# Optimization experiments

Measured on AMD Instinct MI355X. Metric: run time of the kernel, lower is better.

The kernel has to match this reference:

```python
import jax, jax.numpy as jnp
import numpy as np

B, N = 4, 32768
IN_CH, OUT_CH, SD = 4, 4, 3
WIDTH, DEPTH, M, H, FFN = 256, 8, 32, 8, 1024
CF, TF, FB = 8, 4, 1000
IN_DIM = IN_CH + 2 * CF + 2 * TF  # 28
DH = WIDTH // H


def setup_inputs() -> dict:
    key = jax.random.key(0)
    ks = jax.random.split(key, 16)
    r = lambda i, shape, s=0.02: jax.random.normal(ks[i], shape, dtype=jnp.float32) * s
    return {
        "features": jax.random.normal(ks[0], (B, N, IN_CH), dtype=jnp.float32),
        "coords": jax.random.uniform(ks[1], (B, N, SD), minval=-1.0, maxval=1.0),
        "t_norm": jax.random.uniform(ks[2], (B,)),
        "freq_matrix": jax.random.normal(ks[3], (SD, CF), dtype=jnp.float32),
        "omega": FB ** (-jnp.arange(TF, dtype=jnp.float32) / TF),
        "in_w": r(4, (IN_DIM, WIDTH)), "in_b": jnp.zeros((WIDTH,)),
        "ln1_g": jnp.ones((DEPTH, WIDTH)), "ln1_b": jnp.zeros((DEPTH, WIDTH)),
        "slice_w": r(5, (DEPTH, WIDTH, M)), "slice_b": jnp.zeros((DEPTH, M)),
        "qkv_w": r(6, (DEPTH, WIDTH, 3 * WIDTH)), "qkv_b": jnp.zeros((DEPTH, 3 * WIDTH)),
        "attn_out_w": r(7, (DEPTH, WIDTH, WIDTH)), "attn_out_b": jnp.zeros((DEPTH, WIDTH)),
        "ln2_g": jnp.ones((DEPTH, WIDTH)), "ln2_b": jnp.zeros((DEPTH, WIDTH)),
        "ffn1_w": r(8, (DEPTH, WIDTH, FFN)), "ffn1_b": jnp.zeros((DEPTH, FFN)),
        "ffn2_w": r(9, (DEPTH, FFN, WIDTH)), "ffn2_b": jnp.zeros((DEPTH, WIDTH)),
        "out_w": r(10, (WIDTH, OUT_CH)), "out_b": jnp.zeros((OUT_CH,)),
    }


def _ln(x, g, b):
    mu = x.mean(-1, keepdims=True)
    var = ((x - mu) ** 2).mean(-1, keepdims=True)
    return (x - mu) * jax.lax.rsqrt(var + 1e-5) * g + b


def _mha(z, qkv_w, qkv_b, ow, ob):
    # z: (B, M, WIDTH). Standard torch nn.MultiheadAttention self-attn.
    qkv = z @ qkv_w + qkv_b                      # (B, M, 3*WIDTH)
    q, k, v = jnp.split(qkv, 3, axis=-1)
    sh = (z.shape[0], M, H, DH)
    q = q.reshape(sh).transpose(0, 2, 1, 3)      # (B, H, M, DH)
    k = k.reshape(sh).transpose(0, 2, 1, 3)
    v = v.reshape(sh).transpose(0, 2, 1, 3)
    scores = jnp.einsum('bhmd,bhkd->bhmk', q, k) / jnp.sqrt(jnp.float32(DH))
    attn = jax.nn.softmax(scores, axis=-1)
    o = jnp.einsum('bhmk,bhkd->bhmd', attn, v)   # (B, H, M, DH)
    o = o.transpose(0, 2, 1, 3).reshape(z.shape[0], M, WIDTH)
    return o @ ow + ob


def _physics_attention(h, sw, sb, qkv_w, qkv_b, ow, ob):
    # h: (B, N, WIDTH)
    w = jax.nn.softmax(h @ sw + sb, axis=-1)                 # (B, N, M)
    wsum = jnp.clip(w.sum(axis=1), 1e-8, None)               # (B, M)
    slices = jnp.einsum('bnm,bnd->bmd', w, h) / wsum[..., None]
    slices_out = _mha(slices, qkv_w, qkv_b, ow, ob)          # (B, M, WIDTH)
    return jnp.einsum('bnm,bmd->bnd', w, slices_out)         # (B, N, WIDTH)


def _forward(features, coords, t_norm, freq_matrix, omega, in_w, in_b,
             ln1_g, ln1_b, slice_w, slice_b, qkv_w, qkv_b, attn_out_w, attn_out_b,
             ln2_g, ln2_b, ffn1_w, ffn1_b, ffn2_w, ffn2_b, out_w, out_b):
    # Spatial LFF encoding
    proj = 2.0 * jnp.pi * (coords @ freq_matrix)             # (B, N, CF)
    sp = jnp.concatenate([jnp.sin(proj), jnp.cos(proj)], axis=-1)
    # Temporal sinusoidal encoding, broadcast to all nodes
    angles = omega[None, :] * (t_norm * FB)[:, None]         # (B, TF)
    te = jnp.concatenate([jnp.sin(angles), jnp.cos(angles)], axis=-1)
    te = jnp.broadcast_to(te[:, None, :], (features.shape[0], features.shape[1], 2 * TF))
    x = jnp.concatenate([features, sp, te], axis=-1) @ in_w + in_b  # (B, N, WIDTH)
    for i in range(DEPTH):
        h = _ln(x, ln1_g[i], ln1_b[i])
        x = x + _physics_attention(h, slice_w[i], slice_b[i], qkv_w[i], qkv_b[i],
                                   attn_out_w[i], attn_out_b[i])
        h2 = _ln(x, ln2_g[i], ln2_b[i])
        x = x + jax.nn.gelu(h2 @ ffn1_w[i] + ffn1_b[i], approximate=False) @ ffn2_w[i] + ffn2_b[i]
    return x @ out_w + out_b                                 # (B, N, OUT_CH)


def reference(features, coords, t_norm, freq_matrix, omega, in_w, in_b,
              ln1_g, ln1_b, slice_w, slice_b, qkv_w, qkv_b, attn_out_w, attn_out_b,
              ln2_g, ln2_b, ffn1_w, ffn1_b, ffn2_w, ffn2_b, out_w, out_b):
    return _forward(features, coords, t_norm, freq_matrix, omega, in_w, in_b,
                    ln1_g, ln1_b, slice_w, slice_b, qkv_w, qkv_b, attn_out_w, attn_out_b,
                    ln2_g, ln2_b, ffn1_w, ffn1_b, ffn2_w, ffn2_b, out_w, out_b)
```

## Files before the change

### kernel.cpp

```cpp
#include <hip/hip_runtime.h>

#define BB 4
#define NN 32768
#define BN 131072
#define WD 256
#define NDEPTH 8
#define MS 32
#define NH 8
#define DHD 32
#define FF 1024

typedef float f32x4 __attribute__((ext_vector_type(4)));
typedef float f32x2 __attribute__((ext_vector_type(2)));
typedef _Float16 f16x8 __attribute__((ext_vector_type(8)));
typedef _Float16 f16x4 __attribute__((ext_vector_type(4)));

__device__ __forceinline__ float rcp_(float x){ return __builtin_amdgcn_rcpf(x); }
__device__ __forceinline__ float rsq_(float x){ return __builtin_amdgcn_rsqf(x); }

__device__ __forceinline__ float gelu_f(float x){
  float z  = 0.70710678118654752f * x;
  float az = fabsf(z);
  float t  = rcp_(fmaf(0.3275911f, az, 1.0f));
  float p  = fmaf(t, 1.061405429f, -1.453152027f);
  p = fmaf(t, p, 1.421413741f);
  p = fmaf(t, p, -0.284496736f);
  p = fmaf(t, p, 0.254829592f);
  p = p * t;
  float e  = __expf(-az*az);
  float er = 1.0f - p*e;
  er = (z < 0.0f) ? -er : er;
  return 0.5f * x * (1.0f + er);
}

__global__ __launch_bounds__(256) void k_prep_w1t(const float* __restrict__ f1w,
                                                  const float* __restrict__ ln2g,
                                                  _Float16* __restrict__ W1T){
  int id = blockIdx.x*256 + threadIdx.x;
  int k = id & 255; int f = (id >> 8) & 1023; int i = id >> 18;
  W1T[id] = (_Float16)(ln2g[i*256+k] * f1w[(size_t)i*262144 + (size_t)k*1024 + f]);
}
__global__ __launch_bounds__(256) void k_prep_w2t(const float* __restrict__ f2w,
                                                  _Float16* __restrict__ W2T){
  int id = blockIdx.x*256 + threadIdx.x;
  int k = id & 1023; int n = (id >> 10) & 255; int i = id >> 18;
  W2T[id] = (_Float16)(f2w[(size_t)i*262144 + (size_t)k*256 + n]);
}
__global__ __launch_bounds__(256) void k_prep_s1c1(const float* __restrict__ f1w,
                                                   const float* __restrict__ ln2g,
                                                   const float* __restrict__ ln2b,
                                                   const float* __restrict__ f1b,
                                                   float* __restrict__ S1, float* __restrict__ C1){
  int fb = blockIdx.x; int i = blockIdx.y; int t = threadIdx.x;
  int f = fb*256 + t;
  const float* w = f1w + (size_t)i*262144 + f;
  float s = 0.f, c = 0.f;
  for (int k = 0; k < 256; ++k){
    float wv = w[(size_t)k*1024];
    s = fmaf(ln2g[i*256+k], wv, s);
    c = fmaf(ln2b[i*256+k], wv, c);
  }
  S1[i*1024+f] = s;
  C1[i*1024+f] = c + f1b[i*1024+f];
}
__global__ __launch_bounds__(256) void k_prep_qkvt(const float* __restrict__ qkvw,
                                                   float* __restrict__ qkvwT){
  int id = blockIdx.x*256 + threadIdx.x;
  int d = id & 255; int cl = id >> 8;
  int c = cl % 768; int L = cl / 768;
  qkvwT[id] = qkvw[(size_t)L*196608 + (size_t)d*768 + c];
}

__global__ __launch_bounds__(256) void k_encode(const float* __restrict__ feat,
                                                const float* __restrict__ coords,
                                                const float* __restrict__ tn,
                                                const float* __restrict__ fm,
                                                const float* __restrict__ om,
                                                const float* __restrict__ in_w,
                                                const float* __restrict__ in_b,
                                                float* __restrict__ X){
  __shared__ float inw[28*256];
  __shared__ float enc[8][28];
  int t = threadIdx.x;
  for (int i = 0; i < 28; ++i) inw[i*256+t] = in_w[i*256+t];
  float bv = in_b[t];
  int row0 = blockIdx.x * 128;
  __syncthreads();
  for (int it = 0; it < 16; ++it){
    int rbase = row0 + it*8;
    if (t < 224){
      int rr = t / 28, j = t - rr*28;
      int row = rbase + rr; int b = row >> 15;
      float v;
      if (j < 4){
        v = feat[(size_t)row*4 + j];
      } else if (j < 20){
        int fi = (j - 4) & 7;
        const float* cp = coords + (size_t)row*3;
        float pr = 6.2831853071795864f * (cp[0]*fm[fi] + cp[1]*fm[8+fi] + cp[2]*fm[16+fi]);
        v = (j < 12) ? sinf(pr) : cosf(pr);
      } else {
        int fi = (j - 20) & 3;
        float ang = om[fi] * (tn[b] * 1000.0f);
        v = (j < 24) ? sinf(ang) : cosf(ang);
      }
      enc[rr][j] = v;
    }
    __syncthreads();
    for (int rr = 0; rr < 8; ++rr){
      float a = bv;
      #pragma unroll 7
      for (int j = 0; j < 28; ++j) a = fmaf(enc[rr][j], inw[j*256+t], a);
      X[(size_t)(rbase+rr)*256 + t] = a;
    }
    __syncthreads();
  }
}

__global__ __launch_bounds__(256) void k_slice(const float* __restrict__ X,
                                               float* __restrict__ Wb,
                                               float* __restrict__ S,
                                               float* __restrict__ WS,
                                               const float* __restrict__ swp,
                                               const float* __restrict__ sbp,
                                               const float* __restrict__ g1p,
                                               const float* __restrict__ b1p){
  __shared__ float hl[4][256];
  __shared__ float part[4][256];
  __shared__ float wl[4][32];
  __shared__ float red[4][8];
  int t = threadIdx.x;
  int base = (t >> 5) << 5;
  int m = t & 31;
  float swreg[32];
  #pragma unroll
  for (int j = 0; j < 32; ++j) swreg[j] = swp[(size_t)(base+j)*32 + m];
  float g1 = g1p[t], b1 = b1p[t];
  float sbv = sbp[t & 31];
  float acc[32];
  #pragma unroll
  for (int i = 0; i < 32; ++i) acc[i] = 0.f;
  float wacc = 0.f;
  int row0 = blockIdx.x * 128;
  int b = row0 >> 15;
  int wv_id = t >> 6;
  for (int it = 0; it < 32; ++it){
    int rb = row0 + it*4;
    float xv[4], sm[4], qm[4];
    #pragma unroll
    for (int r = 0; r < 4; ++r) xv[r] = X[(size_t)(rb+r)*256 + t];
    #pragma unroll
    for (int r = 0; r < 4; ++r){ sm[r] = xv[r]; qm[r] = xv[r]*xv[r]; }
    #pragma unroll
    for (int off = 32; off; off >>= 1){
      #pragma unroll
      for (int r = 0; r < 4; ++r){ sm[r] += __shfl_xor(sm[r], off); qm[r] += __shfl_xor(qm[r], off); }
    }
    if ((t & 63) == 0){
      #pragma unroll
      for (int r = 0; r < 4; ++r){ red[r][wv_id*2] = sm[r]; red[r][wv_id*2+1] = qm[r]; }
    }
    __syncthreads();
    float h[4];
    #pragma unroll
    for (int r = 0; r < 4; ++r){
      float sum = red[r][0]+red[r][2]+red[r][4]+red[r][6];
      float sq  = red[r][1]+red[r][3]+red[r][5]+red[r][7];
      float mu  = sum * (1.f/256.f);
      float var = sq * (1.f/256.f) - mu*mu;
      float rstd = rsq_(var + 1e-5f);
      h[r] = (xv[r] - mu)*rstd*g1 + b1;
      hl[r][t] = h[r];
    }
    __syncthreads();
    #pragma unroll
    for (int r = 0; r < 4; ++r){
      float p = 0.f;
      #pragma unroll
      for (int j = 0; j < 32; ++j) p = fmaf(hl[r][base+j], swreg[j], p);
      part[r][t] = p;
    }
    __syncthreads();
    if (t < 128){
      int r = t >> 5, mm = t & 31;
      float lg = sbv;
      #pragma unroll
      for (int g = 0; g < 8; ++g) lg += part[r][g*32 + mm];
      float mx = lg;
      #pragma unroll
      for (int off = 16; off; off >>= 1) mx = fmaxf(mx, __shfl_xor(mx, off));
      float e = __expf(lg - mx);
      float se = e;
      #pragma unroll
      for (int off = 16; off; off >>= 1) se += __shfl_xor(se, off);
      float wv = e * rcp_(se);
      wl[r][mm] = wv;
      Wb[(size_t)(rb+r)*32 + mm] = wv;
      wacc += wv;
    }
    __syncthreads();
    #pragma unroll
    for (int r = 0; r < 4; ++r)
      #pragma unroll
      for (int i = 0; i < 32; ++i) acc[i] = fmaf(wl[r][i], h[r], acc[i]);
  }
  #pragma unroll 8
  for (int i = 0; i < 32; ++i) atomicAdd(&S[(size_t)(b*32+i)*256 + t], acc[i]);
  if (t < 128) ((float*)hl)[t] = wacc;
  __syncthreads();
  if (t < 32){
    float* f = (float*)hl;
    atomicAdd(&WS[b*32 + t], f[t] + f[32+t] + f[64+t] + f[96+t]);
  }
}

__global__ __launch_bounds__(256) void k_mha(const float* __restrict__ S,
                                             const float* __restrict__ WS,
                                             float* __restrict__ O,
                                             const float* __restrict__ qkvwT,
                                             const float* __restrict__ qkvb){
  __shared__ float zl[32*256];
  __shared__ float qkl[3][32][33];
  __shared__ float att[32][33];
  __shared__ float wsl[32];
  int t = threadIdx.x;
  int b = blockIdx.x >> 3, h = blockIdx.x & 7;
  if (t < 32) wsl[t] = rcp_(fmaxf(WS[b*32+t], 1e-8f));
  __syncthreads();
  #pragma unroll
  for (int i = 0; i < 8; ++i){
    int idx = i*1024 + t*4;
    int mm = idx >> 8; int d = idx & 255;
    f32x4 v = *reinterpret_cast<const f32x4*>(S + (size_t)(b*32+mm)*256 + d);
    v *= wsl[mm];
    *reinterpret_cast<f32x4*>(&zl[idx]) = v;
  }
  __syncthreads();
  for (int i = 0; i < 12; ++i){
    int o = i*256 + t;
    int which = o >> 10, rem = o & 1023, mm = rem >> 5, dh = rem & 31;
    int col = which*256 + h*32 + dh;
    const f32x4* zp = reinterpret_cast<const f32x4*>(&zl[mm*256]);
    const f32x4* wp = reinterpret_cast<const f32x4*>(qkvwT + (size_t)col*256);
    f32x4 av = {0.f,0.f,0.f,0.f};
    #pragma unroll 8
    for (int d4 = 0; d4 < 64; ++d4) av += zp[d4]*wp[d4];
    qkl[which][mm][dh] = av[0]+av[1]+av[2]+av[3] + qkvb[col];
  }
  __syncthreads();
  for (int i = 0; i < 4; ++i){
    int e = i*256 + t; int mm = e >> 5; int k2 = e & 31;
    float a = 0.f;
    #pragma unroll 8
    for (int d = 0; d < 32; ++d) a = fmaf(qkl[0][mm][d], qkl[1][k2][d], a);
    att[mm][k2] = a * 0.17677669529663687f;
  }
  __syncthreads();
  {
    int mm = t >> 3, j = t & 7;
    float v0 = att[mm][j], v1 = att[mm][j+8], v2 = att[mm][j+16], v3 = att[mm][j+24];
    float mx = fmaxf(fmaxf(v0, v1), fmaxf(v2, v3));
    #pragma unroll
    for (int off = 4; off; off >>= 1) mx = fmaxf(mx, __shfl_xor(mx, off));
    v0 = __expf(v0-mx); v1 = __expf(v1-mx); v2 = __expf(v2-mx); v3 = __expf(v3-mx);
    float sm = v0+v1+v2+v3;
    #pragma unroll
    for (int off = 4; off; off >>= 1) sm += __shfl_xor(sm, off);
    float inv = rcp_(sm);
    att[mm][j] = v0*inv; att[mm][j+8] = v1*inv; att[mm][j+16] = v2*inv; att[mm][j+24] = v3*inv;
  }
  __syncthreads();
  for (int i = 0; i < 4; ++i){
    int e = i*256 + t; int mm = e >> 5; int dh = e & 31;
    float a = 0.f;
    #pragma unroll 8
    for (int k2 = 0; k2 < 32; ++k2) a = fmaf(att[mm][k2], qkl[2][k2][dh], a);
    O[(size_t)(b*32+mm)*256 + h*32 + dh] = a;
  }
}

__global__ __launch_bounds__(256) void k_outproj(const float* __restrict__ O,
                                                 float* __restrict__ SO,
                                                 const float* __restrict__ aow,
                                                 const float* __restrict__ aob){
  __shared__ float orow[256];
  int t = threadIdx.x; int row = blockIdx.x;
  orow[t] = O[(size_t)row*256 + t];
  __syncthreads();
  float a = aob[t];
  #pragma unroll 4
  for (int d = 0; d < 256; ++d) a = fmaf(orow[d], aow[(size_t)d*256 + t], a);
  SO[(size_t)row*256 + t] = a;
}

__global__ __launch_bounds__(256) void k_deslice(float* __restrict__ X,
                                                 const float* __restrict__ Wb,
                                                 const float* __restrict__ SO,
                                                 float* __restrict__ ST){
  __shared__ float wrow[4][32];
  __shared__ float red[4][8];
  int t = threadIdx.x;
  int row0 = blockIdx.x * 32;
  int b = row0 >> 15;
  int wv_id = t >> 6;
  float soc[32];
  #pragma unroll 8
  for (int i = 0; i < 32; ++i) soc[i] = SO[(size_t)(b*32+i)*256 + t];
  for (int it = 0; it < 8; ++it){
    int rb = row0 + it*4;
    if (t < 128) wrow[t>>5][t&31] = Wb[(size_t)(rb + (t>>5))*32 + (t&31)];
    __syncthreads();
    float xn[4], sm[4], qm[4];
    #pragma unroll
    for (int r = 0; r < 4; ++r){
      float xv = X[(size_t)(rb+r)*256 + t];
      float dv = 0.f;
      #pragma unroll
      for (int i = 0; i < 32; ++i) dv = fmaf(wrow[r][i], soc[i], dv);
      xn[r] = xv + dv;
      X[(size_t)(rb+r)*256 + t] = xn[r];
      sm[r] = xn[r]; qm[r] = xn[r]*xn[r];
    }
    #pragma unroll
    for (int off = 32; off; off >>= 1){
      #pragma unroll
      for (int r = 0; r < 4; ++r){ sm[r] += __shfl_xor(sm[r], off); qm[r] += __shfl_xor(qm[r], off); }
    }
    if ((t & 63) == 0){
      #pragma unroll
      for (int r = 0; r < 4; ++r){ red[r][wv_id*2] = sm[r]; red[r][wv_id*2+1] = qm[r]; }
    }
    __syncthreads();
    if (t < 4){
      int r = t;
      float sum = red[r][0]+red[r][2]+red[r][4]+red[r][6];
      float sq  = red[r][1]+red[r][3]+red[r][5]+red[r][7];
      float mu  = sum * (1.f/256.f);
      float var = sq * (1.f/256.f) - mu*mu;
      float rstd = rsq_(var + 1e-5f);
      ST[(size_t)(rb+r)*2]   = rstd;
      ST[(size_t)(rb+r)*2+1] = rstd*mu;
    }
  }
}

__global__ __launch_bounds__(256) void k_ffn1(const float* __restrict__ X,
                                              const _Float16* __restrict__ W1T,
                                              const float* __restrict__ S1,
                                              const float* __restrict__ C1,
                                              const float* __restrict__ ST,
                                              _Float16* __restrict__ U, int c0){
  __shared__ _Float16 As[128*40];
  __shared__ _Float16 Bs[128*40];
  __shared__ f32x2 stl[128];
  int t = threadIdx.x;
  int nb = blockIdx.x;
  int my = blockIdx.y;
  int row0 = c0 + my*128;
  int w = t >> 6, l = t & 63;
  int wm = w >> 1, wn = w & 1, lr = l & 15, lk = l >> 4;
  f32x4 acc[4][4] = {};
  for (int ks = 0; ks < 8; ++ks){
    int k0 = ks*32;
    {
      int r = t >> 3, qd = t & 7;
      #pragma unroll
      for (int i = 0; i < 4; ++i){
        int rr = i*32 + r;
        f32x4 v = *reinterpret_cast<const f32x4*>(X + (size_t)(row0+rr)*256 + k0 + qd*4);
        f16x4 hv; hv[0]=(_Float16)v[0]; hv[1]=(_Float16)v[1]; hv[2]=(_Float16)v[2]; hv[3]=(_Float16)v[3];
        *reinterpret_cast<f16x4*>(&As[rr*40 + qd*4]) = hv;
      }
      #pragma unroll
      for (int i = 0; i < 2; ++i){
        int e = i*256 + t; int fr = e >> 2; int qb = e & 3;
        f16x8 hv = *reinterpret_cast<const f16x8*>(W1T + (size_t)(nb*128+fr)*256 + k0 + qb*8);
        *reinterpret_cast<f16x8*>(&Bs[fr*40 + qb*8]) = hv;
      }
    }
    __syncthreads();
    f16x8 a[4], bf[4];
    #pragma unroll
    for (int i = 0; i < 4; ++i) a[i]  = *reinterpret_cast<const f16x8*>(&As[(64*wm + 16*i + lr)*40 + lk*8]);
    #pragma unroll
    for (int i = 0; i < 4; ++i) bf[i] = *reinterpret_cast<const f16x8*>(&Bs[(64*wn + 16*i + lr)*40 + lk*8]);
    #pragma unroll
    for (int mt = 0; mt < 4; ++mt)
      #pragma unroll
      for (int nt = 0; nt < 4; ++nt)
        acc[mt][nt] = __builtin_amdgcn_mfma_f32_16x16x32_f16(a[mt], bf[nt], acc[mt][nt], 0, 0, 0);
    __syncthreads();
  }
  if (t < 128) stl[t] = *reinterpret_cast<const f32x2*>(ST + (size_t)(row0+t)*2);
  __syncthreads();
  #pragma unroll
  for (int nt = 0; nt < 4; ++nt){
    int f = nb*128 + 64*wn + 16*nt + lr;
    float s1 = S1[f], c1 = C1[f];
    #pragma unroll
    for (int mt = 0; mt < 4; ++mt){
      int lrow0 = 64*wm + 16*mt + lk*4;
      #pragma unroll
      for (int e = 0; e < 4; ++e){
        f32x2 st2 = stl[lrow0 + e];
        float u = st2[0]*acc[mt][nt][e] - st2[1]*s1 + c1;
        U[(size_t)(my*128 + lrow0 + e)*1024 + f] = (_Float16)gelu_f(u);
      }
    }
  }
}

__global__ __launch_bounds__(256) void k_ffn2(const _Float16* __restrict__ U,
                                              const _Float16* __restrict__ W2T,
                                              const float* __restrict__ f2b,
                                              float* __restrict__ X, int c0){
  __shared__ _Float16 As[128*40];
  __shared__ _Float16 Bs[128*40];
  int t = threadIdx.x;
  int nb = blockIdx.x;
  int my = blockIdx.y;
  int w = t >> 6, l = t & 63;
  int wm = w >> 1, wn = w & 1, lr = l & 15, lk = l >> 4;
  f32x4 acc[4][4] = {};
  for (int ks = 0; ks < 32; ++ks){
    int k0 = ks*32;
    #pragma unroll
    for (int i = 0; i < 2; ++i){
      int e = i*256 + t; int r = e >> 2; int qb = e & 3;
      f16x8 hv  = *reinterpret_cast<const f16x8*>(U   + (size_t)(my*128+r)*1024 + k0 + qb*8);
      *reinterpret_cast<f16x8*>(&As[r*40 + qb*8]) = hv;
      f16x8 hv2 = *reinterpret_cast<const f16x8*>(W2T + (size_t)(nb*128+r)*1024 + k0 + qb*8);
      *reinterpret_cast<f16x8*>(&Bs[r*40 + qb*8]) = hv2;
    }
    __syncthreads();
    f16x8 a[4], bf[4];
    #pragma unroll
    for (int i = 0; i < 4; ++i) a[i]  = *reinterpret_cast<const f16x8*>(&As[(64*wm + 16*i + lr)*40 + lk*8]);
    #pragma unroll
    for (int i = 0; i < 4; ++i) bf[i] = *reinterpret_cast<const f16x8*>(&Bs[(64*wn + 16*i + lr)*40 + lk*8]);
    #pragma unroll
    for (int mt = 0; mt < 4; ++mt)
      #pragma unroll
      for (int nt = 0; nt < 4; ++nt)
        acc[mt][nt] = __builtin_amdgcn_mfma_f32_16x16x32_f16(a[mt], bf[nt], acc[mt][nt], 0, 0, 0);
    __syncthreads();
  }
  #pragma unroll
  for (int nt = 0; nt < 4; ++nt){
    int c = nb*128 + 64*wn + 16*nt + lr;
    float bv = f2b[c];
    #pragma unroll
    for (int mt = 0; mt < 4; ++mt){
      int gr = c0 + my*128 + 64*wm + 16*mt + lk*4;
      #pragma unroll
      for (int e = 0; e < 4; ++e){
        size_t idx = (size_t)(gr+e)*256 + c;
        X[idx] = X[idx] + acc[mt][nt][e] + bv;
      }
    }
  }
}

__global__ __launch_bounds__(256) void k_final(const float* __restrict__ X,
                                               const float* __restrict__ out_w,
                                               const float* __restrict__ out_b,
                                               float* __restrict__ out){
  int t = threadIdx.x; int w = t >> 6; int l = t & 63;
  f32x4 ow[4];
  #pragma unroll
  for (int j = 0; j < 4; ++j) ow[j] = *reinterpret_cast<const f32x4*>(out_w + (4*l+j)*4);
  f32x4 ob = *reinterpret_cast<const f32x4*>(out_b);
  int row0 = blockIdx.x * 256;
  for (int it = 0; it < 64; ++it){
    int row = row0 + it*4 + w;
    f32x4 xv = *reinterpret_cast<const f32x4*>(X + (size_t)row*256 + 4*l);
    f32x4 p = ow[0]*xv[0];
    p += ow[1]*xv[1]; p += ow[2]*xv[2]; p += ow[3]*xv[3];
    #pragma unroll
    for (int off = 32; off; off >>= 1){
      p[0] += __shfl_xor(p[0], off);
      p[1] += __shfl_xor(p[1], off);
      p[2] += __shfl_xor(p[2], off);
      p[3] += __shfl_xor(p[3], off);
    }
    if (l == 0) *reinterpret_cast<f32x4*>(out + (size_t)row*4) = p + ob;
  }
}

static constexpr size_t OFF_X   = 0;
static constexpr size_t SZ_X    = (size_t)BN*256*4;
static constexpr size_t OFF_W   = OFF_X + SZ_X;
static constexpr size_t SZ_W    = (size_t)BN*32*4;
static constexpr size_t OFF_ST  = OFF_W + SZ_W;
static constexpr size_t SZ_ST   = (size_t)BN*2*4;
static constexpr size_t OFF_S   = OFF_ST + SZ_ST;
static constexpr size_t SZ_S    = (size_t)4*32*256*4;
static constexpr size_t OFF_WS  = OFF_S + SZ_S;
static constexpr size_t OFF_O   = OFF_WS + 1024;
static constexpr size_t OFF_SO  = OFF_O + 131072;
static constexpr size_t OFF_W1T = OFF_SO + 131072;
static constexpr size_t SZ_W1T  = (size_t)8*1024*256*2;
static constexpr size_t OFF_W2T = OFF_W1T + SZ_W1T;
static constexpr size_t OFF_S1  = OFF_W2T + SZ_W1T;
static constexpr size_t OFF_C1  = OFF_S1 + 8*1024*4;
static constexpr size_t OFF_QT  = OFF_C1 + 8*1024*4;
static constexpr size_t SZ_QT   = (size_t)8*768*256*4;
static constexpr size_t OFF_U   = OFF_QT + SZ_QT;

extern "C" void kernel_launch(void* const* d_in, const int* in_sizes, int n_in,
                              void* d_out, int out_size, void* d_ws, size_t ws_size,
                              hipStream_t stream) {
  (void)in_sizes; (void)n_in; (void)out_size;
  const float* features = (const float*)d_in[0];
  const float* coords   = (const float*)d_in[1];
  const float* t_norm   = (const float*)d_in[2];
  const float* freqm    = (const float*)d_in[3];
  const float* omega    = (const float*)d_in[4];
  const float* in_w     = (const float*)d_in[5];
  const float* in_b     = (const float*)d_in[6];
  const float* ln1_g    = (const float*)d_in[7];
  const float* ln1_b    = (const float*)d_in[8];
  const float* slice_w  = (const float*)d_in[9];
  const float* slice_b  = (const float*)d_in[10];
  const float* qkv_w    = (const float*)d_in[11];
  const float* qkv_b    = (const float*)d_in[12];
  const float* aow      = (const float*)d_in[13];
  const float* aob      = (const float*)d_in[14];
  const float* ln2_g    = (const float*)d_in[15];
  const float* ln2_b    = (const float*)d_in[16];
  const float* f1w      = (const float*)d_in[17];
  const float* f1b      = (const float*)d_in[18];
  const float* f2w      = (const float*)d_in[19];
  const float* f2b      = (const float*)d_in[20];
  const float* out_w    = (const float*)d_in[21];
  const float* out_b    = (const float*)d_in[22];

  char* ws = (char*)d_ws;
  float*     X    = (float*)(ws + OFF_X);
  float*     Wb   = (float*)(ws + OFF_W);
  float*     ST   = (float*)(ws + OFF_ST);
  float*     S    = (float*)(ws + OFF_S);
  float*     WS   = (float*)(ws + OFF_WS);
  float*     O    = (float*)(ws + OFF_O);
  float*     SO   = (float*)(ws + OFF_SO);
  _Float16*  W1T  = (_Float16*)(ws + OFF_W1T);
  _Float16*  W2T  = (_Float16*)(ws + OFF_W2T);
  float*     S1   = (float*)(ws + OFF_S1);
  float*     C1   = (float*)(ws + OFF_C1);
  float*     QT   = (float*)(ws + OFF_QT);
  _Float16*  U    = (_Float16*)(ws + OFF_U);

  int CH = 1;
  while (CH < 32 && OFF_U + (size_t)(BN/CH)*FF*2 > ws_size) CH <<= 1;
  int crows = BN / CH;

  k_prep_w1t<<<8192, 256, 0, stream>>>(f1w, ln2_g, W1T);
  k_prep_w2t<<<8192, 256, 0, stream>>>(f2w, W2T);
  k_prep_s1c1<<<dim3(4, 8), 256, 0, stream>>>(f1w, ln2_g, ln2_b, f1b, S1, C1);
  k_prep_qkvt<<<6144, 256, 0, stream>>>(qkv_w, QT);
  k_encode<<<1024, 256, 0, stream>>>(features, coords, t_norm, freqm, omega, in_w, in_b, X);

  for (int L = 0; L < NDEPTH; ++L){
    hipMemsetAsync(ws + OFF_S, 0, SZ_S + 1024, stream);
    k_slice<<<1024, 256, 0, stream>>>(X, Wb, S, WS,
        slice_w + (size_t)L*8192, slice_b + (size_t)L*32,
        ln1_g + (size_t)L*256, ln1_b + (size_t)L*256);
    k_mha<<<32, 256, 0, stream>>>(S, WS, O,
        QT + (size_t)L*196608, qkv_b + (size_t)L*768);
    k_outproj<<<128, 256, 0, stream>>>(O, SO,
        aow + (size_t)L*65536, aob + (size_t)L*256);
    k_deslice<<<4096, 256, 0, stream>>>(X, Wb, SO, ST);
    for (int c = 0; c < CH; ++c){
      int c0 = c * crows;
      k_ffn1<<<dim3(8, crows/128), 256, 0, stream>>>(X,
          W1T + (size_t)L*262144, S1 + (size_t)L*1024, C1 + (size_t)L*1024, ST, U, c0);
      k_ffn2<<<dim3(2, crows/128), 256, 0, stream>>>(U,
          W2T + (size_t)L*262144, f2b + (size_t)L*256, X, c0);
    }
  }
  k_final<<<512, 256, 0, stream>>>(X, out_w, out_b, (float*)d_out);
}
```

Baseline: 7.315 ms.

## Double-buffer FFN GEMMs with direct global-to-LDS loads and keep fp16 residual copy

Both FFN GEMM kernels now stage tiles with global_load_lds into swizzled, double-buffered shared memory. The next K-slice is prefetched while the current one is multiplied, and one barrier per iteration is dropped. To allow raw fp16 loads for FFN1, encode, deslice and ffn2 also write an fp16 copy of the residual stream (X16), so the fp32-to-fp16 conversion in the FFN1 loader goes away. The slice kernel's LayerNorm is reworked so each wave handles one row with vectorized loads and wave-only reductions, removing a barrier; the cost is an extra 64MB buffer and extra fp16 writes.

New measurement: 8.240 ms. 12.6% more time.

```diff
diff --git a/kernel.cpp b/kernel.cpp
--- a/kernel.cpp
+++ b/kernel.cpp
@@ -78,7 +78,8 @@
                                                 const float* __restrict__ om,
                                                 const float* __restrict__ in_w,
                                                 const float* __restrict__ in_b,
-                                                float* __restrict__ X){
+                                                float* __restrict__ X,
+                                                _Float16* __restrict__ X16){
   __shared__ float inw[28*256];
   __shared__ float enc[8][28];
   int t = threadIdx.x;
@@ -112,6 +113,7 @@
       #pragma unroll 7
       for (int j = 0; j < 28; ++j) a = fmaf(enc[rr][j], inw[j*256+t], a);
       X[(size_t)(rbase+rr)*256 + t] = a;
+      X16[(size_t)(rbase+rr)*256 + t] = (_Float16)a;
     }
     __syncthreads();
   }
@@ -128,51 +130,41 @@
   __shared__ float hl[4][256];
   __shared__ float part[4][256];
   __shared__ float wl[4][32];
-  __shared__ float red[4][8];
   int t = threadIdx.x;
+  int wv = t >> 6, l = t & 63;
   int base = (t >> 5) << 5;
   int m = t & 31;
   float swreg[32];
   #pragma unroll
   for (int j = 0; j < 32; ++j) swreg[j] = swp[(size_t)(base+j)*32 + m];
-  float g1 = g1p[t], b1 = b1p[t];
-  float sbv = sbp[t & 31];
+  f32x4 g4 = *reinterpret_cast<const f32x4*>(g1p + 4*l);
+  f32x4 b4 = *reinterpret_cast<const f32x4*>(b1p + 4*l);
+  float sbv = sbp[m];
   float acc[32];
   #pragma unroll
   for (int i = 0; i < 32; ++i) acc[i] = 0.f;
   float wacc = 0.f;
   int row0 = blockIdx.x * 128;
   int b = row0 >> 15;
-  int wv_id = t >> 6;
   for (int it = 0; it < 32; ++it){
     int rb = row0 + it*4;
-    float xv[4], sm[4], qm[4];
-    #pragma unroll
-    for (int r = 0; r < 4; ++r) xv[r] = X[(size_t)(rb+r)*256 + t];
-    #pragma unroll
-    for (int r = 0; r < 4; ++r){ sm[r] = xv[r]; qm[r] = xv[r]*xv[r]; }
-    #pragma unroll
-    for (int off = 32; off; off >>= 1){
-      #pragma unroll
-      for (int r = 0; r < 4; ++r){ sm[r] += __shfl_xor(sm[r], off); qm[r] += __shfl_xor(qm[r], off); }
-    }
-    if ((t & 63) == 0){
-      #pragma unroll
-      for (int r = 0; r < 4; ++r){ red[r][wv_id*2] = sm[r]; red[r][wv_id*2+1] = qm[r]; }
-    }
-    __syncthreads();
-    float h[4];
-    #pragma unroll
-    for (int r = 0; r < 4; ++r){
-      float sum = red[r][0]+red[r][2]+red[r][4]+red[r][6];
-      float sq  = red[r][1]+red[r][3]+red[r][5]+red[r][7];
-      float mu  = sum * (1.f/256.f);
-      float var = sq * (1.f/256.f) - mu*mu;
-      float rstd = rsq_(var + 1e-5f);
-      h[r] = (xv[r] - mu)*rstd*g1 + b1;
-      hl[r][t] = h[r];
-    }
-    __syncthreads();
+    int row = rb + wv;
+    f32x4 xv = *reinterpret_cast<const f32x4*>(X + (size_t)row*256 + 4*l);
+    float s = xv[0]+xv[1]+xv[2]+xv[3];
+    float q = xv[0]*xv[0]+xv[1]*xv[1]+xv[2]*xv[2]+xv[3]*xv[3];
+    #pragma unroll
+    for (int off = 32; off; off >>= 1){ s += __shfl_xor(s, off); q += __shfl_xor(q, off); }
+    float mu  = s * (1.f/256.f);
+    float var = q * (1.f/256.f) - mu*mu;
+    float rstd = rsq_(var + 1e-5f);
+    f32x4 h4;
+    #pragma unroll
+    for (int j = 0; j < 4; ++j) h4[j] = (xv[j] - mu)*rstd*g4[j] + b4[j];
+    *reinterpret_cast<f32x4*>(&hl[wv][4*l]) = h4;
+    __syncthreads();
+    float hc[4];
+    #pragma unroll
+    for (int r = 0; r < 4; ++r) hc[r] = hl[r][t];
     #pragma unroll
     for (int r = 0; r < 4; ++r){
       float p = 0.f;
@@ -193,16 +185,16 @@
       float se = e;
       #pragma unroll
       for (int off = 16; off; off >>= 1) se += __shfl_xor(se, off);
-      float wv = e * rcp_(se);
-      wl[r][mm] = wv;
-      Wb[(size_t)(rb+r)*32 + mm] = wv;
-      wacc += wv;
+      float wvv = e * rcp_(se);
+      wl[r][mm] = wvv;
+      Wb[(size_t)(rb+r)*32 + mm] = wvv;
+      wacc += wvv;
     }
     __syncthreads();
     #pragma unroll
     for (int r = 0; r < 4; ++r)
       #pragma unroll
-      for (int i = 0; i < 32; ++i) acc[i] = fmaf(wl[r][i], h[r], acc[i]);
+      for (int i = 0; i < 32; ++i) acc[i] = fmaf(wl[r][i], hc[r], acc[i]);
   }
   #pragma unroll 8
   for (int i = 0; i < 32; ++i) atomicAdd(&S[(size_t)(b*32+i)*256 + t], acc[i]);
@@ -294,6 +286,7 @@
 }
 
 __global__ __launch_bounds__(256) void k_deslice(float* __restrict__ X,
+                                                 _Float16* __restrict__ X16,
                                                  const float* __restrict__ Wb,
                                                  const float* __restrict__ SO,
                                                  float* __restrict__ ST){
@@ -319,6 +312,7 @@
       for (int i = 0; i < 32; ++i) dv = fmaf(wrow[r][i], soc[i], dv);
       xn[r] = xv + dv;
       X[(size_t)(rb+r)*256 + t] = xn[r];
+      X16[(size_t)(rb+r)*256 + t] = (_Float16)xn[r];
       sm[r] = xn[r]; qm[r] = xn[r]*xn[r];
     }
     #pragma unroll
@@ -344,52 +338,53 @@
   }
 }
 
-__global__ __launch_bounds__(256) void k_ffn1(const float* __restrict__ X,
+__global__ __launch_bounds__(256) void k_ffn1(const _Float16* __restrict__ X16,
                                               const _Float16* __restrict__ W1T,
                                               const float* __restrict__ S1,
                                               const float* __restrict__ C1,
                                               const float* __restrict__ ST,
                                               _Float16* __restrict__ U, int c0){
-  __shared__ _Float16 As[128*40];
-  __shared__ _Float16 Bs[128*40];
+  __shared__ __align__(16) _Float16 As[2][4096];
+  __shared__ __align__(16) _Float16 Bs[2][4096];
   __shared__ f32x2 stl[128];
   int t = threadIdx.x;
-  int nb = blockIdx.x;
-  int my = blockIdx.y;
-  int row0 = c0 + my*128;
   int w = t >> 6, l = t & 63;
   int wm = w >> 1, wn = w & 1, lr = l & 15, lk = l >> 4;
+  int nb = blockIdx.x, my = blockIdx.y;
+  int row0 = c0 + my*128;
+  int col0 = nb*128;
+  int schunk = ((l&3) ^ ((l>>3)&3)) * 8;
+  int rslot  = (lk ^ ((lr>>1)&3)) * 8;
+  const _Float16* ga = X16 + (size_t)(row0 + w*32 + (l>>2))*256 + schunk;
+  const _Float16* gb = W1T + (size_t)(col0 + w*32 + (l>>2))*256 + schunk;
   f32x4 acc[4][4] = {};
+  #pragma unroll
+  for (int j = 0; j < 2; ++j){
+    __builtin_amdgcn_global_load_lds(ga + (size_t)j*16*256, &As[0][w*1024 + j*512], 16, 0, 0);
+    __builtin_amdgcn_global_load_lds(gb + (size_t)j*16*256, &Bs[0][w*1024 + j*512], 16, 0, 0);
+  }
+  int buf = 0;
   for (int ks = 0; ks < 8; ++ks){
-    int k0 = ks*32;
-    {
-      int r = t >> 3, qd = t & 7;
-      #pragma unroll
-      for (int i = 0; i < 4; ++i){
-        int rr = i*32 + r;
-        f32x4 v = *reinterpret_cast<const f32x4*>(X + (size_t)(row0+rr)*256 + k0 + qd*4);
-        f16x4 hv; hv[0]=(_Float16)v[0]; hv[1]=(_Float16)v[1]; hv[2]=(_Float16)v[2]; hv[3]=(_Float16)v[3];
-        *reinterpret_cast<f16x4*>(&As[rr*40 + qd*4]) = hv;
+    __syncthreads();
+    if (ks < 7){
+      int k0 = (ks+1)*32;
+      #pragma unroll
+      for (int j = 0; j < 2; ++j){
+        __builtin_amdgcn_global_load_lds(ga + k0 + (size_t)j*16*256, &As[buf^1][w*1024 + j*512], 16, 0, 0);
+        __builtin_amdgcn_global_load_lds(gb + k0 + (size_t)j*16*256, &Bs[buf^1][w*1024 + j*512], 16, 0, 0);
       }
-      #pragma unroll
-      for (int i = 0; i < 2; ++i){
-        int e = i*256 + t; int fr = e >> 2; int qb = e & 3;
-        f16x8 hv = *reinterpret_cast<const f16x8*>(W1T + (size_t)(nb*128+fr)*256 + k0 + qb*8);
-        *reinterpret_cast<f16x8*>(&Bs[fr*40 + qb*8]) = hv;
-      }
-    }
-    __syncthreads();
-    f16x8 a[4], bf[4];
-    #pragma unroll
-    for (int i = 0; i < 4; ++i) a[i]  = *reinterpret_cast<const f16x8*>(&As[(64*wm + 16*i + lr)*40 + lk*8]);
-    #pragma unroll
-    for (int i = 0; i < 4; ++i) bf[i] = *reinterpret_cast<const f16x8*>(&Bs[(64*wn + 16*i + lr)*40 + lk*8]);
+    }
+    f16x8 a[4], bfr[4];
+    #pragma unroll
+    for (int i = 0; i < 4; ++i) a[i]   = *reinterpret_cast<const f16x8*>(&As[buf][(64*wm + 16*i + lr)*32 + rslot]);
+    #pragma unroll
+    for (int i = 0; i < 4; ++i) bfr[i] = *reinterpret_cast<const f16x8*>(&Bs[buf][(64*wn + 16*i + lr)*32 + rslot]);
     #pragma unroll
     for (int mt = 0; mt < 4; ++mt)
       #pragma unroll
       for (int nt = 0; nt < 4; ++nt)
-        acc[mt][nt] = __builtin_amdgcn_mfma_f32_16x16x32_f16(a[mt], bf[nt], acc[mt][nt], 0, 0, 0);
-    __syncthreads();
+        acc[mt][nt] = __builtin_amdgcn_mfma_f32_16x16x32_f16(a[mt], bfr[nt], acc[mt][nt], 0, 0, 0);
+    buf ^= 1;
   }
   if (t < 128) stl[t] = *reinterpret_cast<const f32x2*>(ST + (size_t)(row0+t)*2);
   __syncthreads();
@@ -413,37 +408,47 @@
 __global__ __launch_bounds__(256) void k_ffn2(const _Float16* __restrict__ U,
                                               const _Float16* __restrict__ W2T,
                                               const float* __restrict__ f2b,
-                                              float* __restrict__ X, int c0){
-  __shared__ _Float16 As[128*40];
-  __shared__ _Float16 Bs[128*40];
+                                              float* __restrict__ X,
+                                              _Float16* __restrict__ X16, int c0){
+  __shared__ __align__(16) _Float16 As[2][4096];
+  __shared__ __align__(16) _Float16 Bs[2][4096];
   int t = threadIdx.x;
-  int nb = blockIdx.x;
-  int my = blockIdx.y;
   int w = t >> 6, l = t & 63;
   int wm = w >> 1, wn = w & 1, lr = l & 15, lk = l >> 4;
+  int nb = blockIdx.x, my = blockIdx.y;
+  int col0 = nb*128;
+  int schunk = ((l&3) ^ ((l>>3)&3)) * 8;
+  int rslot  = (lk ^ ((lr>>1)&3)) * 8;
+  const _Float16* ga = U   + (size_t)(my*128 + w*32 + (l>>2))*1024 + schunk;
+  const _Float16* gb = W2T + (size_t)(col0   + w*32 + (l>>2))*1024 + schunk;
   f32x4 acc[4][4] = {};
+  #pragma unroll
+  for (int j = 0; j < 2; ++j){
+    __builtin_amdgcn_global_load_lds(ga + (size_t)j*16*1024, &As[0][w*1024 + j*512], 16, 0, 0);
+    __builtin_amdgcn_global_load_lds(gb + (size_t)j*16*1024, &Bs[0][w*1024 + j*512], 16, 0, 0);
+  }
+  int buf = 0;
   for (int ks = 0; ks < 32; ++ks){
-    int k0 = ks*32;
-    #pragma unroll
-    for (int i = 0; i < 2; ++i){
-      int e = i*256 + t; int r = e >> 2; int qb = e & 3;
-      f16x8 hv  = *reinterpret_cast<const f16x8*>(U   + (size_t)(my*128+r)*1024 + k0 + qb*8);
-      *reinterpret_cast<f16x8*>(&As[r*40 + qb*8]) = hv;
-      f16x8 hv2 = *reinterpret_cast<const f16x8*>(W2T + (size_t)(nb*128+r)*1024 + k0 + qb*8);
-      *reinterpret_cast<f16x8*>(&Bs[r*40 + qb*8]) = hv2;
-    }
-    __syncthreads();
-    f16x8 a[4], bf[4];
-    #pragma unroll
-    for (int i = 0; i < 4; ++i) a[i]  = *reinterpret_cast<const f16x8*>(&As[(64*wm + 16*i + lr)*40 + lk*8]);
-    #pragma unroll
-    for (int i = 0; i < 4; ++i) bf[i] = *reinterpret_cast<const f16x8*>(&Bs[(64*wn + 16*i + lr)*40 + lk*8]);
+    __syncthreads();
+    if (ks < 31){
+      int k0 = (ks+1)*32;
+      #pragma unroll
+      for (int j = 0; j < 2; ++j){
+        __builtin_amdgcn_global_load_lds(ga + k0 + (size_t)j*16*1024, &As[buf^1][w*1024 + j*512], 16, 0, 0);
+        __builtin_amdgcn_global_load_lds(gb + k0 + (size_t)j*16*1024, &Bs[buf^1][w*1024 + j*512], 16, 0, 0);
+      }
+    }
+    f16x8 a[4], bfr[4];
+    #pragma unroll
+    for (int i = 0; i < 4; ++i) a[i]   = *reinterpret_cast<const f16x8*>(&As[buf][(64*wm + 16*i + lr)*32 + rslot]);
+    #pragma unroll
+    for (int i = 0; i < 4; ++i) bfr[i] = *reinterpret_cast<const f16x8*>(&Bs[buf][(64*wn + 16*i + lr)*32 + rslot]);
     #pragma unroll
     for (int mt = 0; mt < 4; ++mt)
       #pragma unroll
       for (int nt = 0; nt < 4; ++nt)
-        acc[mt][nt] = __builtin_amdgcn_mfma_f32_16x16x32_f16(a[mt], bf[nt], acc[mt][nt], 0, 0, 0);
-    __syncthreads();
+        acc[mt][nt] = __builtin_amdgcn_mfma_f32_16x16x32_f16(a[mt], bfr[nt], acc[mt][nt], 0, 0, 0);
+    buf ^= 1;
   }
   #pragma unroll
   for (int nt = 0; nt < 4; ++nt){
@@ -455,7 +460,9 @@
       #pragma unroll
       for (int e = 0; e < 4; ++e){
         size_t idx = (size_t)(gr+e)*256 + c;
-        X[idx] = X[idx] + acc[mt][nt][e] + bv;
+        float xn = X[idx] + acc[mt][nt][e] + bv;
+        X[idx] = xn;
+        X16[idx] = (_Float16)xn;
       }
     }
   }
@@ -505,7 +512,9 @@
 static constexpr size_t OFF_C1  = OFF_S1 + 8*1024*4;
 static constexpr size_t OFF_QT  = OFF_C1 + 8*1024*4;
 static constexpr size_t SZ_QT   = (size_t)8*768*256*4;
-static constexpr size_t OFF_U   = OFF_QT + SZ_QT;
+static constexpr size_t OFF_X16 = OFF_QT + SZ_QT;
+static constexpr size_t SZ_X16  = (size_t)BN*256*2;
+static constexpr size_t OFF_U   = OFF_X16 + SZ_X16;
 
 extern "C" void kernel_launch(void* const* d_in, const int* in_sizes, int n_in,
                               void* d_out, int out_size, void* d_ws, size_t ws_size,
@@ -548,6 +557,7 @@
   float*     S1   = (float*)(ws + OFF_S1);
   float*     C1   = (float*)(ws + OFF_C1);
   float*     QT   = (float*)(ws + OFF_QT);
+  _Float16*  X16  = (_Float16*)(ws + OFF_X16);
   _Float16*  U    = (_Float16*)(ws + OFF_U);
 
   int CH = 1;
@@ -558,7 +568,7 @@
   k_prep_w2t<<<8192, 256, 0, stream>>>(f2w, W2T);
   k_prep_s1c1<<<dim3(4, 8), 256, 0, stream>>>(f1w, ln2_g, ln2_b, f1b, S1, C1);
   k_prep_qkvt<<<6144, 256, 0, stream>>>(qkv_w, QT);
-  k_encode<<<1024, 256, 0, stream>>>(features, coords, t_norm, freqm, omega, in_w, in_b, X);
+  k_encode<<<1024, 256, 0, stream>>>(features, coords, t_norm, freqm, omega, in_w, in_b, X, X16);
 
   for (int L = 0; L < NDEPTH; ++L){
     hipMemsetAsync(ws + OFF_S, 0, SZ_S + 1024, stream);
@@ -569,13 +579,13 @@
         QT + (size_t)L*196608, qkv_b + (size_t)L*768);
     k_outproj<<<128, 256, 0, stream>>>(O, SO,
         aow + (size_t)L*65536, aob + (size_t)L*256);
-    k_deslice<<<4096, 256, 0, stream>>>(X, Wb, SO, ST);
+    k_deslice<<<4096, 256, 0, stream>>>(X, X16, Wb, SO, ST);
     for (int c = 0; c < CH; ++c){
       int c0 = c * crows;
-      k_ffn1<<<dim3(8, crows/128), 256, 0, stream>>>(X,
+      k_ffn1<<<dim3(8, crows/128), 256, 0, stream>>>(X16,
           W1T + (size_t)L*262144, S1 + (size_t)L*1024, C1 + (size_t)L*1024, ST, U, c0);
       k_ffn2<<<dim3(2, crows/128), 256, 0, stream>>>(U,
-          W2T + (size_t)L*262144, f2b + (size_t)L*256, X, c0);
+          W2T + (size_t)L*262144, f2b + (size_t)L*256, X, X16, c0);
     }
   }
   k_final<<<512, 256, 0, stream>>>(X, out_w, out_b, (float*)d_out);
```
